# Optimization experiments

Measured on AMD Instinct MI355X. Metric: run time of the kernel, lower is better.

The kernel has to match this reference:

```python
import jax, jax.numpy as jnp
import numpy as np

N_SUB = 16
IN, OUT, WIDTH, DEPTH = 1, 1, 128, 4  # DEPTH-1 hidden->hidden layers
EPS = 1e-8
FT = 0.3  # fixed_transition
N_PTS = 65536


def setup_inputs() -> dict:
    key = jax.random.key(0)
    ks = jax.random.split(key, 8)
    x = jax.random.uniform(ks[0], (N_PTS, IN), dtype=jnp.float32)

    # overlapping subdomains tiling [0,1]
    i = jnp.arange(N_SUB, dtype=jnp.float32)
    xmins = (i / N_SUB - 0.05)[:, None]          # (S, 1)
    xmaxs = ((i + 1) / N_SUB + 0.05)[:, None]    # (S, 1)
    t = jnp.log((1 - EPS) / EPS)
    w = jnp.full_like(xmins, FT)
    mu_min = xmins + w / 2
    sd_min = w / (2 * t)
    mu_max = xmaxs - w / 2
    sd_max = w / (2 * t)
    centres = (xmins + xmaxs) / 2
    scales = (xmaxs - xmins) / 2

    s_in = 1.0 / np.sqrt(IN)
    s_h = 1.0 / np.sqrt(WIDTH)
    W0 = jax.random.normal(ks[1], (N_SUB, WIDTH, IN), jnp.float32) * s_in
    b0 = jnp.zeros((N_SUB, WIDTH), jnp.float32)
    Wh = jax.random.normal(ks[2], (N_SUB, DEPTH - 1, WIDTH, WIDTH), jnp.float32) * s_h
    bh = jnp.zeros((N_SUB, DEPTH - 1, WIDTH), jnp.float32)
    Wout = jax.random.normal(ks[3], (N_SUB, OUT, WIDTH), jnp.float32) * s_h
    bout = jnp.zeros((N_SUB, OUT), jnp.float32)

    return dict(x=x, W0=W0, b0=b0, Wh=Wh, bh=bh, Wout=Wout, bout=bout,
                centres=centres, scales=scales,
                mu_min=mu_min, sd_min=sd_min, mu_max=mu_max, sd_max=sd_max)


def reference(x, W0, b0, Wh, bh, Wout, bout, centres, scales,
              mu_min, sd_min, mu_max, sd_max):
    # window weights: partition-of-unity sigmoids on first coordinate  (S, N)
    x0 = x[None, :, 0]                                   # (1, N)
    w_lo = jax.nn.sigmoid((x0 - mu_min[:, 0:1]) / sd_min[:, 0:1])
    w_hi = jax.nn.sigmoid((mu_max[:, 0:1] - x0) / sd_max[:, 0:1])
    wm = w_lo * w_hi                                     # (S, N)

    # per-subnet normalised inputs  (S, N, IN)
    xi = (x[None, :, :] - centres[:, None, :]) / jnp.maximum(scales, EPS)[:, None, :]

    # batched small MLP over subnets (tanh hidden, linear head)
    h = jnp.tanh(jnp.einsum('swi,sni->snw', W0, xi) + b0[:, None, :])
    for l in range(DEPTH - 1):
        h = jnp.tanh(jnp.einsum('svw,snw->snv', Wh[:, l], h) + bh[:, l, None, :])
    raw = (jnp.einsum('sow,snw->sno', Wout, h) + bout[:, None, :])[..., 0]  # (S, N)

    # windowed sum over subnets -> (N, 1)
    return jnp.sum(wm * raw, axis=0)[:, None]
```

## Files before the change

kernel.cpp:

```cpp
#include <hip/hip_runtime.h>
#include <hip/hip_bf16.h>
#include <math.h>

#define NPTS   65536
#define NS     16
#define WID    128
#define NHID   3
#define CAP    24576
#define CZ     -25.33f
#define CSTR   32

#define OFF_IDX 2048
#define OFF_WF  (OFF_IDX + NS * CAP * 4)
#define OFF_WO  (OFF_WF + NS * NHID * WID * WID * 2)

typedef _Float16 f16x8 __attribute__((ext_vector_type(8)));
typedef _Float16 f16x4 __attribute__((ext_vector_type(4)));
typedef float    f32x4 __attribute__((ext_vector_type(4)));

__device__ __forceinline__ float tanh5(float x) {
    float e = __builtin_amdgcn_exp2f(x * 2.8853900817779268f);
    float r = __builtin_amdgcn_rcpf(e + 1.f);
    return fmaf(-2.f, r, 1.f);
}
__device__ __forceinline__ float sigmf(float z) {
    float e = __builtin_amdgcn_exp2f(-z * 1.4426950408889634f);
    return __builtin_amdgcn_rcpf(1.f + e);
}

__global__ void init_kernel(int* __restrict__ counts,
                            const float* __restrict__ Wh, _Float16* __restrict__ WF,
                            const float* __restrict__ Wout, _Float16* __restrict__ WoutF) {
    int b = blockIdx.x, t = threadIdx.x;
    if (b == 0 && t < NS) counts[t * CSTR] = 0;
    if (b < 384) {
        int g = b * 256 + t;
        int sl = g >> 11, r = g & 2047;
        int vt = r >> 8, kk = (r >> 6) & 3, lane = r & 63;
        int v = vt * 16 + (lane & 15);
        int w0 = kk * 32 + (lane >> 4) * 8;
        const float* src = Wh + (sl << 14) + v * WID + w0;
        float4 a = *(const float4*)src;
        float4 c = *(const float4*)(src + 4);
        f16x8 o;
        o[0] = (_Float16)a.x; o[1] = (_Float16)a.y; o[2] = (_Float16)a.z; o[3] = (_Float16)a.w;
        o[4] = (_Float16)c.x; o[5] = (_Float16)c.y; o[6] = (_Float16)c.z; o[7] = (_Float16)c.w;
        ((f16x8*)WF)[g] = o;
    } else {
        int g = (b - 384) * 256 + t;
        int s = g >> 8, kk = (g >> 6) & 3, lane = g & 63;
        f16x8 o = (f16x8)(_Float16)0.f;
        if ((lane & 15) == 0) {
            int w0 = kk * 32 + (lane >> 4) * 8;
            const float* src = Wout + s * WID + w0;
            float4 a = *(const float4*)src;
            float4 c = *(const float4*)(src + 4);
            o[0] = (_Float16)a.x; o[1] = (_Float16)a.y; o[2] = (_Float16)a.z; o[3] = (_Float16)a.w;
            o[4] = (_Float16)c.x; o[5] = (_Float16)c.y; o[6] = (_Float16)c.z; o[7] = (_Float16)c.w;
        }
        ((f16x8*)WoutF)[g] = o;
    }
}

__global__ void bucket_kernel(const float* __restrict__ x,
                              const float* __restrict__ mu_min, const float* __restrict__ sd_min,
                              const float* __restrict__ mu_max, const float* __restrict__ sd_max,
                              int* counts, int* __restrict__ idx,
                              float* __restrict__ out) {
    __shared__ int wcnt[NS][4];
    __shared__ int wbase[NS][4];
    __shared__ int bbase[NS];
    int t = threadIdx.x, lane = t & 63, wid = t >> 6;
    int n = blockIdx.x * 256 + t;
    float xv = x[n];
    out[n] = 0.f;
    unsigned long long ltmask = (1ULL << lane) - 1ULL;
    unsigned mbits = 0;
    #pragma unroll
    for (int s = 0; s < NS; ++s) {
        float z1 = __fdividef(xv - mu_min[s], sd_min[s]);
        float z2 = __fdividef(mu_max[s] - xv, sd_max[s]);
        bool m = (z1 > CZ) && (z2 > CZ);
        mbits |= (unsigned)m << s;
        unsigned long long mk = __ballot(m);
        if (lane == 0) wcnt[s][wid] = __popcll(mk);
    }
    __syncthreads();
    if (t < NS) {
        int c0 = wcnt[t][0], c1 = wcnt[t][1], c2 = wcnt[t][2], c3 = wcnt[t][3];
        wbase[t][0] = 0; wbase[t][1] = c0; wbase[t][2] = c0 + c1; wbase[t][3] = c0 + c1 + c2;
        bbase[t] = atomicAdd(&counts[t * CSTR], c0 + c1 + c2 + c3);
    }
    __syncthreads();
    #pragma unroll
    for (int s = 0; s < NS; ++s) {
        bool m = (mbits >> s) & 1;
        unsigned long long mk = __ballot(m);
        if (m) {
            int pos = __popcll(mk & ltmask);
            int g = bbase[s] + wbase[s][wid] + pos;
            if (g < CAP) idx[s * CAP + g] = n;
        }
    }
}

__global__ __launch_bounds__(256, 5) void mlp_kernel(
        const float* __restrict__ x,
        const float* __restrict__ W0,   const float* __restrict__ b0,
        const _Float16* __restrict__ WF, const float* __restrict__ bh,
        const _Float16* __restrict__ WoutF, const float* __restrict__ bout,
        const float* __restrict__ centres, const float* __restrict__ scales,
        const float* __restrict__ mu_min,  const float* __restrict__ sd_min,
        const float* __restrict__ mu_max,  const float* __restrict__ sd_max,
        const int* __restrict__ counts, const int* __restrict__ idx,
        float* __restrict__ out) {
    __shared__ __align__(16) char scr[4][4096];

    int s = blockIdx.x;
    int cnt = counts[s * CSTR]; if (cnt > CAP) cnt = CAP;
    int t = threadIdx.x, lane = t & 63, w = t >> 6;
    int base = blockIdx.y * 64 + w * 16;
    if (base >= cnt) return;
    int g = lane >> 4, p = lane & 15;
    int swz = (p & 7) << 4;
    char* S = scr[w];

    int slot = base + p;
    bool live = slot < cnt;
    int n = 0; float xi = 0.f, wmv = 0.f;
    if (live) {
        n = idx[s * CAP + slot];
        float xv = x[n];
        float wl = sigmf(__fdividef(xv - mu_min[s], sd_min[s]));
        float wh = sigmf(__fdividef(mu_max[s] - xv, sd_max[s]));
        wmv = wl * wh;
        xi = __fdividef(xv - centres[s], fmaxf(scales[s], 1e-8f));
    }

    f16x8 B[4];
    const float* W0p = W0 + s * WID;
    const float* b0p = b0 + s * WID;
    #pragma unroll
    for (int kk = 0; kk < 4; ++kk) {
        int v0 = kk * 32 + g * 8;
        float4 wa = *(const float4*)(W0p + v0), wb = *(const float4*)(W0p + v0 + 4);
        float4 ba = *(const float4*)(b0p + v0), bb = *(const float4*)(b0p + v0 + 4);
        f16x8 hv;
        hv[0] = (_Float16)tanh5(fmaf(wa.x, xi, ba.x));
        hv[1] = (_Float16)tanh5(fmaf(wa.y, xi, ba.y));
        hv[2] = (_Float16)tanh5(fmaf(wa.z, xi, ba.z));
        hv[3] = (_Float16)tanh5(fmaf(wa.w, xi, ba.w));
        hv[4] = (_Float16)tanh5(fmaf(wb.x, xi, bb.x));
        hv[5] = (_Float16)tanh5(fmaf(wb.y, xi, bb.y));
        hv[6] = (_Float16)tanh5(fmaf(wb.z, xi, bb.z));
        hv[7] = (_Float16)tanh5(fmaf(wb.w, xi, bb.w));
        B[kk] = hv;
    }

    for (int l = 0; l < NHID; ++l) {
        const f16x8* WFp = (const f16x8*)WF + (size_t)(s * NHID + l) * 2048;
        const float* bhp = bh + (s * NHID + l) * WID;
        f32x4 acc[8];
        #pragma unroll
        for (int vt = 0; vt < 8; ++vt) {
            f32x4 a = *(const f32x4*)(bhp + vt * 16 + g * 4);
            #pragma unroll
            for (int kk = 0; kk < 4; ++kk) {
                f16x8 af = WFp[(vt * 4 + kk) * 64 + lane];
                a = __builtin_amdgcn_mfma_f32_16x16x32_f16(af, B[kk], a, 0, 0, 0);
            }
            acc[vt] = a;
        }
        #pragma unroll
        for (int vt = 0; vt < 8; ++vt) {
            f16x4 q;
            q[0] = (_Float16)tanh5(acc[vt][0]);
            q[1] = (_Float16)tanh5(acc[vt][1]);
            q[2] = (_Float16)tanh5(acc[vt][2]);
            q[3] = (_Float16)tanh5(acc[vt][3]);
            *(f16x4*)(S + p * 256 + ((((g * 4 + vt * 16) * 2)) ^ swz)) = q;
        }
        #pragma unroll
        for (int kk = 0; kk < 4; ++kk)
            B[kk] = *(const f16x8*)(S + p * 256 + ((((kk * 32 + g * 8) * 2)) ^ swz));
    }

    {
        float bo = bout[s];
        f32x4 oacc = (f32x4){bo, bo, bo, bo};
        const f16x8* WOp = (const f16x8*)WoutF + s * 256;
        #pragma unroll
        for (int kk = 0; kk < 4; ++kk)
            oacc = __builtin_amdgcn_mfma_f32_16x16x32_f16(WOp[kk * 64 + lane], B[kk], oacc, 0, 0, 0);
        if (g == 0 && live) atomicAdd(&out[n], wmv * oacc[0]);
    }
}

extern "C" void kernel_launch(void* const* d_in, const int* in_sizes, int n_in,
                              void* d_out, int out_size, void* d_ws, size_t ws_size,
                              hipStream_t stream) {
    const float* x       = (const float*)d_in[0];
    const float* W0      = (const float*)d_in[1];
    const float* b0      = (const float*)d_in[2];
    const float* Wh      = (const float*)d_in[3];
    const float* bh      = (const float*)d_in[4];
    const float* Wout    = (const float*)d_in[5];
    const float* bout    = (const float*)d_in[6];
    const float* centres = (const float*)d_in[7];
    const float* scales  = (const float*)d_in[8];
    const float* mu_min  = (const float*)d_in[9];
    const float* sd_min  = (const float*)d_in[10];
    const float* mu_max  = (const float*)d_in[11];
    const float* sd_max  = (const float*)d_in[12];
    float* out = (float*)d_out;
    char* ws = (char*)d_ws;
    int*      counts = (int*)ws;
    int*      idx    = (int*)(ws + OFF_IDX);
    _Float16* WF     = (_Float16*)(ws + OFF_WF);
    _Float16* WoutF  = (_Float16*)(ws + OFF_WO);

    init_kernel<<<dim3(400), dim3(256), 0, stream>>>(counts, Wh, WF, Wout, WoutF);
    bucket_kernel<<<dim3(NPTS / 256), dim3(256), 0, stream>>>(x, mu_min, sd_min, mu_max, sd_max,
                                                              counts, idx, out);
    dim3 grid(NS, CAP / 64);
    mlp_kernel<<<grid, dim3(256), 0, stream>>>(x, W0, b0, WF, bh, WoutF, bout,
                                               centres, scales, mu_min, sd_min, mu_max, sd_max,
                                               counts, idx, out);
}
```

Measured before the change: 173.8 us.

## Process 64 points per wave to reuse weight fragments; merge prep kernels

Each wave now handles four 16-point groups, so every weight fragment loaded from global memory feeds four MFMAs instead of one. Hidden activations are ping-ponged between two register sets, with an LDS transpose done per pair of output tiles. The init and bucket kernels are merged into one launch, and the counter reset moves to a memset. Register pressure rises sharply (launch bounds drop to 2 blocks per CU), which lowers occupancy and the number of blocks in the grid.

```diff
diff --git a/kernel.cpp b/kernel.cpp
--- a/kernel.cpp
+++ b/kernel.cpp
@@ -28,13 +28,51 @@
     return __builtin_amdgcn_rcpf(1.f + e);
 }
 
-__global__ void init_kernel(int* __restrict__ counts,
+__global__ void prep_kernel(const float* __restrict__ x,
+                            const float* __restrict__ mu_min, const float* __restrict__ sd_min,
+                            const float* __restrict__ mu_max, const float* __restrict__ sd_max,
+                            int* counts, int* __restrict__ idx, float* __restrict__ out,
                             const float* __restrict__ Wh, _Float16* __restrict__ WF,
                             const float* __restrict__ Wout, _Float16* __restrict__ WoutF) {
+    __shared__ int wcnt[NS][4];
+    __shared__ int wbase[NS][4];
+    __shared__ int bbase[NS];
     int b = blockIdx.x, t = threadIdx.x;
-    if (b == 0 && t < NS) counts[t * CSTR] = 0;
-    if (b < 384) {
-        int g = b * 256 + t;
+    if (b < 256) {
+        int lane = t & 63, wid = t >> 6;
+        int n = b * 256 + t;
+        float xv = x[n];
+        out[n] = 0.f;
+        unsigned long long ltmask = (1ULL << lane) - 1ULL;
+        unsigned mbits = 0;
+        #pragma unroll
+        for (int s = 0; s < NS; ++s) {
+            float z1 = __fdividef(xv - mu_min[s], sd_min[s]);
+            float z2 = __fdividef(mu_max[s] - xv, sd_max[s]);
+            bool m = (z1 > CZ) && (z2 > CZ);
+            mbits |= (unsigned)m << s;
+            unsigned long long mk = __ballot(m);
+            if (lane == 0) wcnt[s][wid] = __popcll(mk);
+        }
+        __syncthreads();
+        if (t < NS) {
+            int c0 = wcnt[t][0], c1 = wcnt[t][1], c2 = wcnt[t][2], c3 = wcnt[t][3];
+            wbase[t][0] = 0; wbase[t][1] = c0; wbase[t][2] = c0 + c1; wbase[t][3] = c0 + c1 + c2;
+            bbase[t] = atomicAdd(&counts[t * CSTR], c0 + c1 + c2 + c3);
+        }
+        __syncthreads();
+        #pragma unroll
+        for (int s = 0; s < NS; ++s) {
+            bool m = (mbits >> s) & 1;
+            unsigned long long mk = __ballot(m);
+            if (m) {
+                int pos = __popcll(mk & ltmask);
+                int g = bbase[s] + wbase[s][wid] + pos;
+                if (g < CAP) idx[s * CAP + g] = n;
+            }
+        }
+    } else if (b < 640) {
+        int g = (b - 256) * 256 + t;
         int sl = g >> 11, r = g & 2047;
         int vt = r >> 8, kk = (r >> 6) & 3, lane = r & 63;
         int v = vt * 16 + (lane & 15);
@@ -47,7 +85,7 @@
         o[4] = (_Float16)c.x; o[5] = (_Float16)c.y; o[6] = (_Float16)c.z; o[7] = (_Float16)c.w;
         ((f16x8*)WF)[g] = o;
     } else {
-        int g = (b - 384) * 256 + t;
+        int g = (b - 640) * 256 + t;
         int s = g >> 8, kk = (g >> 6) & 3, lane = g & 63;
         f16x8 o = (f16x8)(_Float16)0.f;
         if ((lane & 15) == 0) {
@@ -62,49 +100,44 @@
     }
 }
 
-__global__ void bucket_kernel(const float* __restrict__ x,
-                              const float* __restrict__ mu_min, const float* __restrict__ sd_min,
-                              const float* __restrict__ mu_max, const float* __restrict__ sd_max,
-                              int* counts, int* __restrict__ idx,
-                              float* __restrict__ out) {
-    __shared__ int wcnt[NS][4];
-    __shared__ int wbase[NS][4];
-    __shared__ int bbase[NS];
-    int t = threadIdx.x, lane = t & 63, wid = t >> 6;
-    int n = blockIdx.x * 256 + t;
-    float xv = x[n];
-    out[n] = 0.f;
-    unsigned long long ltmask = (1ULL << lane) - 1ULL;
-    unsigned mbits = 0;
+__device__ __forceinline__ void layer_body(const f16x8* __restrict__ WFp,
+                                           const float* __restrict__ bhp,
+                                           char* Sw, int lane, int g,
+                                           const int (&wof)[4], const int (&rof)[4],
+                                           const f16x8 (&Bin)[4][4], f16x8 (&Bout)[4][4]) {
     #pragma unroll
-    for (int s = 0; s < NS; ++s) {
-        float z1 = __fdividef(xv - mu_min[s], sd_min[s]);
-        float z2 = __fdividef(mu_max[s] - xv, sd_max[s]);
-        bool m = (z1 > CZ) && (z2 > CZ);
-        mbits |= (unsigned)m << s;
-        unsigned long long mk = __ballot(m);
-        if (lane == 0) wcnt[s][wid] = __popcll(mk);
-    }
-    __syncthreads();
-    if (t < NS) {
-        int c0 = wcnt[t][0], c1 = wcnt[t][1], c2 = wcnt[t][2], c3 = wcnt[t][3];
-        wbase[t][0] = 0; wbase[t][1] = c0; wbase[t][2] = c0 + c1; wbase[t][3] = c0 + c1 + c2;
-        bbase[t] = atomicAdd(&counts[t * CSTR], c0 + c1 + c2 + c3);
-    }
-    __syncthreads();
-    #pragma unroll
-    for (int s = 0; s < NS; ++s) {
-        bool m = (mbits >> s) & 1;
-        unsigned long long mk = __ballot(m);
-        if (m) {
-            int pos = __popcll(mk & ltmask);
-            int g = bbase[s] + wbase[s][wid] + pos;
-            if (g < CAP) idx[s * CAP + g] = n;
-        }
-    }
-}
-
-__global__ __launch_bounds__(256, 5) void mlp_kernel(
+    for (int vt = 0; vt < 8; ++vt) {
+        f32x4 bias = *(const f32x4*)(bhp + vt * 16 + g * 4);
+        f16x8 af[4];
+        #pragma unroll
+        for (int kk = 0; kk < 4; ++kk) af[kk] = WFp[(vt * 4 + kk) * 64 + lane];
+        f32x4 acc[4];
+        #pragma unroll
+        for (int pg = 0; pg < 4; ++pg) acc[pg] = bias;
+        #pragma unroll
+        for (int kk = 0; kk < 4; ++kk)
+            #pragma unroll
+            for (int pg = 0; pg < 4; ++pg)
+                acc[pg] = __builtin_amdgcn_mfma_f32_16x16x32_f16(af[kk], Bin[pg][kk], acc[pg], 0, 0, 0);
+        #pragma unroll
+        for (int pg = 0; pg < 4; ++pg) {
+            f16x4 q;
+            q[0] = (_Float16)tanh5(acc[pg][0]);
+            q[1] = (_Float16)tanh5(acc[pg][1]);
+            q[2] = (_Float16)tanh5(acc[pg][2]);
+            q[3] = (_Float16)tanh5(acc[pg][3]);
+            *(f16x4*)(Sw + ((vt & 1) << 11) + wof[pg]) = q;
+        }
+        if (vt & 1) {
+            const int kk = vt >> 1;
+            #pragma unroll
+            for (int pg = 0; pg < 4; ++pg)
+                Bout[pg][kk] = *(const f16x8*)(Sw + rof[pg]);
+        }
+    }
+}
+
+__global__ __launch_bounds__(256, 2) void mlp_kernel(
         const float* __restrict__ x,
         const float* __restrict__ W0,   const float* __restrict__ b0,
         const _Float16* __restrict__ WF, const float* __restrict__ bh,
@@ -116,83 +149,89 @@
         float* __restrict__ out) {
     __shared__ __align__(16) char scr[4][4096];
 
-    int s = blockIdx.x;
+    int s = blockIdx.y;
     int cnt = counts[s * CSTR]; if (cnt > CAP) cnt = CAP;
     int t = threadIdx.x, lane = t & 63, w = t >> 6;
-    int base = blockIdx.y * 64 + w * 16;
-    if (base >= cnt) return;
+    int wslot0 = blockIdx.x * 256 + w * 64;
+    if (wslot0 >= cnt) return;
     int g = lane >> 4, p = lane & 15;
-    int swz = (p & 7) << 4;
-    char* S = scr[w];
-
-    int slot = base + p;
-    bool live = slot < cnt;
-    int n = 0; float xi = 0.f, wmv = 0.f;
-    if (live) {
-        n = idx[s * CAP + slot];
-        float xv = x[n];
-        float wl = sigmf(__fdividef(xv - mu_min[s], sd_min[s]));
-        float wh = sigmf(__fdividef(mu_max[s] - xv, sd_max[s]));
-        wmv = wl * wh;
-        xi = __fdividef(xv - centres[s], fmaxf(scales[s], 1e-8f));
-    }
-
-    f16x8 B[4];
-    const float* W0p = W0 + s * WID;
-    const float* b0p = b0 + s * WID;
+    char* Sw = scr[w];
+
+    int wof[4], rof[4];
     #pragma unroll
-    for (int kk = 0; kk < 4; ++kk) {
-        int v0 = kk * 32 + g * 8;
-        float4 wa = *(const float4*)(W0p + v0), wb = *(const float4*)(W0p + v0 + 4);
-        float4 ba = *(const float4*)(b0p + v0), bb = *(const float4*)(b0p + v0 + 4);
-        f16x8 hv;
-        hv[0] = (_Float16)tanh5(fmaf(wa.x, xi, ba.x));
-        hv[1] = (_Float16)tanh5(fmaf(wa.y, xi, ba.y));
-        hv[2] = (_Float16)tanh5(fmaf(wa.z, xi, ba.z));
-        hv[3] = (_Float16)tanh5(fmaf(wa.w, xi, ba.w));
-        hv[4] = (_Float16)tanh5(fmaf(wb.x, xi, bb.x));
-        hv[5] = (_Float16)tanh5(fmaf(wb.y, xi, bb.y));
-        hv[6] = (_Float16)tanh5(fmaf(wb.z, xi, bb.z));
-        hv[7] = (_Float16)tanh5(fmaf(wb.w, xi, bb.w));
-        B[kk] = hv;
-    }
-
-    for (int l = 0; l < NHID; ++l) {
-        const f16x8* WFp = (const f16x8*)WF + (size_t)(s * NHID + l) * 2048;
-        const float* bhp = bh + (s * NHID + l) * WID;
-        f32x4 acc[8];
-        #pragma unroll
-        for (int vt = 0; vt < 8; ++vt) {
-            f32x4 a = *(const f32x4*)(bhp + vt * 16 + g * 4);
-            #pragma unroll
-            for (int kk = 0; kk < 4; ++kk) {
-                f16x8 af = WFp[(vt * 4 + kk) * 64 + lane];
-                a = __builtin_amdgcn_mfma_f32_16x16x32_f16(af, B[kk], a, 0, 0, 0);
+    for (int pg = 0; pg < 4; ++pg) {
+        int pt = pg * 16 + p;
+        int sw = ((pt >> 2) & 1) << 4;
+        wof[pg] = pt * 32 + ((g * 8) ^ sw);
+        rof[pg] = ((g >> 1) << 11) + pt * 32 + (((g & 1) * 16) ^ sw);
+    }
+
+    int   n[4]; float wmv[4], xi[4];
+    #pragma unroll
+    for (int pg = 0; pg < 4; ++pg) {
+        int slot = wslot0 + pg * 16 + p;
+        float xiv = 0.f, wv = 0.f; int nn = 0;
+        if (slot < cnt) {
+            nn = idx[s * CAP + slot];
+            float xv = x[nn];
+            float wl = sigmf(__fdividef(xv - mu_min[s], sd_min[s]));
+            float wh = sigmf(__fdividef(mu_max[s] - xv, sd_max[s]));
+            wv = wl * wh;
+            xiv = __fdividef(xv - centres[s], fmaxf(scales[s], 1e-8f));
+        }
+        n[pg] = nn; wmv[pg] = wv; xi[pg] = xiv;
+    }
+
+    f16x8 Ba[4][4], Bb[4][4];
+    {
+        const float* W0p = W0 + s * WID;
+        const float* b0p = b0 + s * WID;
+        #pragma unroll
+        for (int kk = 0; kk < 4; ++kk) {
+            int v0 = kk * 32 + g * 8;
+            float4 wa = *(const float4*)(W0p + v0), wb = *(const float4*)(W0p + v0 + 4);
+            float4 ba = *(const float4*)(b0p + v0), bb = *(const float4*)(b0p + v0 + 4);
+            #pragma unroll
+            for (int pg = 0; pg < 4; ++pg) {
+                float xiv = xi[pg];
+                f16x8 hv;
+                hv[0] = (_Float16)tanh5(fmaf(wa.x, xiv, ba.x));
+                hv[1] = (_Float16)tanh5(fmaf(wa.y, xiv, ba.y));
+                hv[2] = (_Float16)tanh5(fmaf(wa.z, xiv, ba.z));
+                hv[3] = (_Float16)tanh5(fmaf(wa.w, xiv, ba.w));
+                hv[4] = (_Float16)tanh5(fmaf(wb.x, xiv, bb.x));
+                hv[5] = (_Float16)tanh5(fmaf(wb.y, xiv, bb.y));
+                hv[6] = (_Float16)tanh5(fmaf(wb.z, xiv, bb.z));
+                hv[7] = (_Float16)tanh5(fmaf(wb.w, xiv, bb.w));
+                Ba[pg][kk] = hv;
             }
-            acc[vt] = a;
-        }
-        #pragma unroll
-        for (int vt = 0; vt < 8; ++vt) {
-            f16x4 q;
-            q[0] = (_Float16)tanh5(acc[vt][0]);
-            q[1] = (_Float16)tanh5(acc[vt][1]);
-            q[2] = (_Float16)tanh5(acc[vt][2]);
-            q[3] = (_Float16)tanh5(acc[vt][3]);
-            *(f16x4*)(S + p * 256 + ((((g * 4 + vt * 16) * 2)) ^ swz)) = q;
-        }
-        #pragma unroll
-        for (int kk = 0; kk < 4; ++kk)
-            B[kk] = *(const f16x8*)(S + p * 256 + ((((kk * 32 + g * 8) * 2)) ^ swz));
-    }
+        }
+    }
+
+    const f16x8* WF8 = (const f16x8*)WF;
+    const float* bh0 = bh + s * NHID * WID;
+    layer_body(WF8 + (size_t)(s * NHID + 0) * 2048, bh0,           Sw, lane, g, wof, rof, Ba, Bb);
+    layer_body(WF8 + (size_t)(s * NHID + 1) * 2048, bh0 + WID,     Sw, lane, g, wof, rof, Bb, Ba);
+    layer_body(WF8 + (size_t)(s * NHID + 2) * 2048, bh0 + 2 * WID, Sw, lane, g, wof, rof, Ba, Bb);
 
     {
+        const f16x8* WOp = (const f16x8*)WoutF + s * 256;
         float bo = bout[s];
-        f32x4 oacc = (f32x4){bo, bo, bo, bo};
-        const f16x8* WOp = (const f16x8*)WoutF + s * 256;
-        #pragma unroll
-        for (int kk = 0; kk < 4; ++kk)
-            oacc = __builtin_amdgcn_mfma_f32_16x16x32_f16(WOp[kk * 64 + lane], B[kk], oacc, 0, 0, 0);
-        if (g == 0 && live) atomicAdd(&out[n], wmv * oacc[0]);
+        f32x4 oc[4];
+        #pragma unroll
+        for (int pg = 0; pg < 4; ++pg) oc[pg] = (f32x4){bo, bo, bo, bo};
+        #pragma unroll
+        for (int kk = 0; kk < 4; ++kk) {
+            f16x8 a = WOp[kk * 64 + lane];
+            #pragma unroll
+            for (int pg = 0; pg < 4; ++pg)
+                oc[pg] = __builtin_amdgcn_mfma_f32_16x16x32_f16(a, Bb[pg][kk], oc[pg], 0, 0, 0);
+        }
+        if (g == 0) {
+            #pragma unroll
+            for (int pg = 0; pg < 4; ++pg)
+                if (wmv[pg] > 0.f) atomicAdd(&out[n[pg]], wmv[pg] * oc[pg][0]);
+        }
     }
 }
 
@@ -219,10 +258,10 @@
     _Float16* WF     = (_Float16*)(ws + OFF_WF);
     _Float16* WoutF  = (_Float16*)(ws + OFF_WO);
 
-    init_kernel<<<dim3(400), dim3(256), 0, stream>>>(counts, Wh, WF, Wout, WoutF);
-    bucket_kernel<<<dim3(NPTS / 256), dim3(256), 0, stream>>>(x, mu_min, sd_min, mu_max, sd_max,
-                                                              counts, idx, out);
-    dim3 grid(NS, CAP / 64);
+    hipMemsetAsync(counts, 0, NS * CSTR * sizeof(int), stream);
+    prep_kernel<<<dim3(656), dim3(256), 0, stream>>>(x, mu_min, sd_min, mu_max, sd_max,
+                                                     counts, idx, out, Wh, WF, Wout, WoutF);
+    dim3 grid(CAP / 256, NS);
     mlp_kernel<<<grid, dim3(256), 0, stream>>>(x, W0, b0, WF, bh, WoutF, bout,
                                                centres, scales, mu_min, sd_min, mu_max, sd_max,
                                                counts, idx, out);
```

After: 162.5 us. 6.5% less time.
